# Kernel optimization log

Measured on AMD Instinct MI355X. Metric: run time of the kernel, lower is better.

## Reference

```python
import jax, jax.numpy as jnp
import numpy as np
import math

B, N, C, H, CH = 4, 1024, 512, 8, 64  # batch, seq (Q=K), model dim, heads, head dim

def setup_inputs() -> dict:
    key = jax.random.key(0)
    ks = jax.random.split(key, 11)
    s = 0.02  # small init scale for weights
    f32 = jnp.float32
    return {
        "q_x": jax.random.normal(ks[0], (B, N, C), f32),
        "kv_x": jax.random.normal(ks[1], (B, N, C), f32),
        "bias_mask": jax.random.normal(ks[2], (B, 1, 1, N), f32),
        "bias_pair": jax.random.normal(ks[3], (1, H, N, N), f32),
        "Wq": (jax.random.normal(ks[4], (C, H * CH), f32) * s),
        "Wk": (jax.random.normal(ks[5], (C, H * CH), f32) * s),
        "Wv": (jax.random.normal(ks[6], (C, H * CH), f32) * s),
        "Wg": (jax.random.normal(ks[7], (C, H * CH), f32) * s),
        "bg": jnp.ones((H * CH,), f32),           # 'gating' init: bias=1
        "Wo": (jax.random.normal(ks[8], (H * CH, C), f32) * s),
        "bo": jnp.zeros((C,), f32),               # 'final' init
    }

def reference(q_x, kv_x, bias_mask, bias_pair, Wq, Wk, Wv, Wg, bg, Wo, bo):
    inv_sqrt = 1.0 / math.sqrt(CH)
    # projections -> [B, N, H, CH]
    q = (q_x @ Wq).reshape(B, N, H, CH) * inv_sqrt
    k = (kv_x @ Wk).reshape(B, N, H, CH)
    v = (kv_x @ Wv).reshape(B, N, H, CH)
    # scores [B, H, Q, K] with additive broadcast biases
    scores = jnp.einsum("bqhc,bkhc->bhqk", q, k) + bias_mask + bias_pair
    a = jax.nn.softmax(scores, axis=-1)
    o = jnp.einsum("bhqk,bkhc->bqhc", a, v)  # [B, Q, H, CH]
    # gated output
    g = jax.nn.sigmoid(q_x @ Wg + bg).reshape(B, N, H, CH)
    o = o * g
    out = o.reshape(B, N, H * CH) @ Wo + bo  # [B, Q, C]
    return out
```

## Files before the change

kernel.cpp:

```cpp
#include <hip/hip_runtime.h>
#include <hip/hip_bf16.h>
#include <hip/hip_fp16.h>

#define B_ 4
#define N_ 1024
#define C_ 512
#define H_ 8
#define CH_ 64

typedef _Float16 f16x8 __attribute__((ext_vector_type(8)));
typedef _Float16 f16x4 __attribute__((ext_vector_type(4)));
typedef float f32x4 __attribute__((ext_vector_type(4)));

__global__ void cvt_f32_f16(const float* __restrict__ xq, const float* __restrict__ xkv,
                            _Float16* __restrict__ oq, _Float16* __restrict__ okv) {
  const int n4 = (B_ * N_ * C_) / 4;
  int stride = gridDim.x * blockDim.x;
  for (int idx = blockIdx.x * blockDim.x + threadIdx.x; idx < 2 * n4; idx += stride) {
    const float4* src = (idx < n4) ? (const float4*)xq : (const float4*)xkv;
    _Float16* dst = (idx < n4) ? oq : okv;
    int j = (idx < n4) ? idx : idx - n4;
    float4 v = src[j];
    f16x4 h;
    h[0] = (_Float16)v.x; h[1] = (_Float16)v.y;
    h[2] = (_Float16)v.z; h[3] = (_Float16)v.w;
    *(f16x4*)(dst + (size_t)j * 4) = h;
  }
}

__global__ void transpose_w(const float* __restrict__ Wq, const float* __restrict__ Wk,
                            const float* __restrict__ Wv, const float* __restrict__ Wg,
                            const float* __restrict__ Wo, _Float16* __restrict__ WT) {
  int s = blockIdx.z;
  const float* W = (s == 0) ? Wq : (s == 1) ? Wk : (s == 2) ? Wv : (s == 3) ? Wg : Wo;
  __shared__ float tile[32][33];
  int tx = threadIdx.x & 31, ty = threadIdx.x >> 5;
  int k0 = blockIdx.x * 32, n0 = blockIdx.y * 32;
  #pragma unroll
  for (int r = 0; r < 32; r += 8)
    tile[ty + r][tx] = W[(size_t)(k0 + ty + r) * C_ + n0 + tx];
  __syncthreads();
  _Float16* dst = WT + (size_t)s * C_ * C_;
  #pragma unroll
  for (int r = 0; r < 32; r += 8)
    dst[(size_t)(n0 + ty + r) * C_ + k0 + tx] = (_Float16)tile[tx][ty + r];
}

__global__ __launch_bounds__(256, 2) void proj_gemm(
    const _Float16* __restrict__ xq16, const _Float16* __restrict__ xkv16,
    const _Float16* __restrict__ WT, const float* __restrict__ bg,
    _Float16* __restrict__ Qb, _Float16* __restrict__ Kb,
    _Float16* __restrict__ Vt, float* __restrict__ Gb) {
  int nt0 = blockIdx.x * 128;
  int m0 = blockIdx.y * 128;
  int sel = nt0 >> 9;
  int n0 = nt0 & 511;
  const _Float16* X = (sel == 0 || sel == 3) ? xq16 : xkv16;
  const _Float16* Wt = WT + (size_t)sel * C_ * C_;

  __shared__ __align__(16) char lds[32768];
  char* ldsA = lds;
  char* ldsB = lds + 16384;

  int tid = threadIdx.x;
  int lane = tid & 63, w = tid >> 6;
  int wr = w >> 1, wc = w & 1;
  int lr = lane & 15, lg = lane >> 4;

  f32x4 acc[4][4];
  #pragma unroll
  for (int i = 0; i < 4; i++)
    #pragma unroll
    for (int j = 0; j < 4; j++)
      #pragma unroll
      for (int r = 0; r < 4; r++) acc[i][j][r] = 0.f;

  int srow = tid >> 3, scol = tid & 7;

  for (int k0 = 0; k0 < C_; k0 += 64) {
    __syncthreads();
    #pragma unroll
    for (int p = 0; p < 4; p++) {
      int r = p * 32 + srow;
      *(f16x8*)(ldsA + ((r * 128 + scol * 16) ^ ((r & 7) << 4))) =
          *(const f16x8*)(X + (size_t)(m0 + r) * C_ + k0 + scol * 8);
      *(f16x8*)(ldsB + ((r * 128 + scol * 16) ^ ((r & 7) << 4))) =
          *(const f16x8*)(Wt + (size_t)(n0 + r) * C_ + k0 + scol * 8);
    }
    __syncthreads();
    #pragma unroll
    for (int kh = 0; kh < 2; kh++) {
      f16x8 a[4], b[4];
      #pragma unroll
      for (int i = 0; i < 4; i++) {
        int row = wr * 64 + i * 16 + lr;
        a[i] = *(const f16x8*)(ldsA + ((row * 128 + kh * 64 + lg * 16) ^ ((row & 7) << 4)));
        int col = wc * 64 + i * 16 + lr;
        b[i] = *(const f16x8*)(ldsB + ((col * 128 + kh * 64 + lg * 16) ^ ((col & 7) << 4)));
      }
      #pragma unroll
      for (int i = 0; i < 4; i++)
        #pragma unroll
        for (int j = 0; j < 4; j++)
          acc[i][j] = __builtin_amdgcn_mfma_f32_16x16x32_f16(a[i], b[j], acc[i][j], 0, 0, 0);
    }
  }

  const float inv_sqrt = 0.125f;
  #pragma unroll
  for (int i = 0; i < 4; i++) {
    int token = m0 + wr * 64 + i * 16 + lg * 4;
    #pragma unroll
    for (int j = 0; j < 4; j++) {
      int col = n0 + wc * 64 + j * 16 + lr;
      f32x4 v = acc[i][j];
      if (sel == 0) {
        #pragma unroll
        for (int r = 0; r < 4; r++)
          Qb[(size_t)(token + r) * C_ + col] = (_Float16)(v[r] * inv_sqrt);
      } else if (sel == 1) {
        #pragma unroll
        for (int r = 0; r < 4; r++)
          Kb[(size_t)(token + r) * C_ + col] = (_Float16)v[r];
      } else if (sel == 2) {
        int bb = token >> 10;
        int nn = token & 1023;
        int hh = col >> 6, ch = col & 63;
        f16x4 pk;
        #pragma unroll
        for (int r = 0; r < 4; r++) pk[r] = (_Float16)v[r];
        *(f16x4*)(Vt + (size_t)((bb * H_ + hh) * CH_ + ch) * N_ + nn) = pk;
      } else {
        #pragma unroll
        for (int r = 0; r < 4; r++) {
          float x = v[r] + bg[col];
          Gb[(size_t)(token + r) * C_ + col] = 1.f / (1.f + __expf(-x));
        }
      }
    }
  }
}

__global__ __launch_bounds__(256, 2) void attn(
    const _Float16* __restrict__ Qb, const _Float16* __restrict__ Kb,
    const _Float16* __restrict__ Vt, const float* __restrict__ Gb,
    const float* __restrict__ bias_mask, const float* __restrict__ bias_pair,
    _Float16* __restrict__ Ob) {
  int bid = blockIdx.x;
  int b = bid & 3, h = (bid >> 2) & 7, qt = bid >> 5;
  int q0 = qt * 64;
  int tid = threadIdx.x, lane = tid & 63, w = tid >> 6;
  int lr = lane & 15, lg = lane >> 4;

  __shared__ __align__(16) char lds[49152];
  char* ldsK = lds;
  char* ldsV = lds + 16384;
  char* ldsP = lds + 32768;

  f16x8 qf[2];
  {
    int token = b * N_ + q0 + w * 16 + lr;
    const _Float16* qp = Qb + (size_t)token * C_ + h * CH_;
    qf[0] = *(const f16x8*)(qp + lg * 8);
    qf[1] = *(const f16x8*)(qp + 32 + lg * 8);
  }

  f32x4 acc_o[4];
  #pragma unroll
  for (int j = 0; j < 4; j++)
    #pragma unroll
    for (int r = 0; r < 4; r++) acc_o[j][r] = 0.f;
  float m_run[4], l_run[4];
  #pragma unroll
  for (int r = 0; r < 4; r++) { m_run[r] = -1e30f; l_run[r] = 0.f; }

  int srow = tid >> 3, scol = tid & 7;
  int vrow = tid >> 4, vcol = tid & 15;

  for (int kt = 0; kt < 8; kt++) {
    __syncthreads();
    #pragma unroll
    for (int p = 0; p < 4; p++) {
      int r = p * 32 + srow;
      *(f16x8*)(ldsK + ((r * 128 + scol * 16) ^ ((r & 7) << 4))) =
          *(const f16x8*)(Kb + (size_t)(b * N_ + kt * 128 + r) * C_ + h * CH_ + scol * 8);
    }
    #pragma unroll
    for (int p = 0; p < 4; p++) {
      int r = p * 16 + vrow;
      *(f16x8*)(ldsV + ((r * 256 + vcol * 16) ^ ((r & 7) << 4))) =
          *(const f16x8*)(Vt + (size_t)((b * H_ + h) * CH_ + r) * N_ + kt * 128 + vcol * 8);
    }
    __syncthreads();

    f32x4 s[8];
    #pragma unroll
    for (int ct = 0; ct < 8; ct++) {
      #pragma unroll
      for (int r = 0; r < 4; r++) s[ct][r] = 0.f;
      #pragma unroll
      for (int kh = 0; kh < 2; kh++) {
        int row = ct * 16 + lr;
        f16x8 kf = *(const f16x8*)(ldsK + ((row * 128 + kh * 64 + lg * 16) ^ ((row & 7) << 4)));
        s[ct] = __builtin_amdgcn_mfma_f32_16x16x32_f16(qf[kh], kf, s[ct], 0, 0, 0);
      }
    }
    int qrow = q0 + w * 16 + lg * 4;
    #pragma unroll
    for (int ct = 0; ct < 8; ct++) {
      float bm = bias_mask[b * N_ + kt * 128 + ct * 16 + lr];
      const float* bp = bias_pair + ((size_t)h * N_ + qrow) * N_ + kt * 128 + ct * 16 + lr;
      #pragma unroll
      for (int r = 0; r < 4; r++) s[ct][r] += bm + bp[(size_t)r * N_];
    }
    #pragma unroll
    for (int r = 0; r < 4; r++) {
      float mx = s[0][r];
      #pragma unroll
      for (int ct = 1; ct < 8; ct++) mx = fmaxf(mx, s[ct][r]);
      #pragma unroll
      for (int o = 1; o < 16; o <<= 1) mx = fmaxf(mx, __shfl_xor(mx, o, 64));
      float m_new = fmaxf(m_run[r], mx);
      float sc = __expf(m_run[r] - m_new);
      m_run[r] = m_new;
      float sum = 0.f;
      #pragma unroll
      for (int ct = 0; ct < 8; ct++) {
        float p = __expf(s[ct][r] - m_new);
        s[ct][r] = p;
        sum += p;
      }
      #pragma unroll
      for (int o = 1; o < 16; o <<= 1) sum += __shfl_xor(sum, o, 64);
      l_run[r] = l_run[r] * sc + sum;
      #pragma unroll
      for (int j = 0; j < 4; j++) acc_o[j][r] *= sc;
    }
    char* myP = ldsP + w * 4096;
    #pragma unroll
    for (int ct = 0; ct < 8; ct++) {
      #pragma unroll
      for (int r = 0; r < 4; r++) {
        int row = lg * 4 + r;
        *(_Float16*)(myP + ((row * 256 + (ct * 16 + lr) * 2) ^ ((row & 7) << 4))) =
            (_Float16)s[ct][r];
      }
    }
    #pragma unroll
    for (int ks = 0; ks < 4; ks++) {
      f16x8 pf = *(const f16x8*)(myP + ((lr * 256 + ks * 64 + lg * 16) ^ ((lr & 7) << 4)));
      #pragma unroll
      for (int cc = 0; cc < 4; cc++) {
        int vr = cc * 16 + lr;
        f16x8 vf = *(const f16x8*)(ldsV + ((vr * 256 + ks * 64 + lg * 16) ^ ((vr & 7) << 4)));
        acc_o[cc] = __builtin_amdgcn_mfma_f32_16x16x32_f16(pf, vf, acc_o[cc], 0, 0, 0);
      }
    }
  }

  #pragma unroll
  for (int cc = 0; cc < 4; cc++) {
    #pragma unroll
    for (int r = 0; r < 4; r++) {
      int token = b * N_ + q0 + w * 16 + lg * 4 + r;
      int col = h * CH_ + cc * 16 + lr;
      float o = acc_o[cc][r] / l_run[r];
      float gv = Gb[(size_t)token * C_ + col];
      Ob[(size_t)token * C_ + col] = (_Float16)(o * gv);
    }
  }
}

__global__ __launch_bounds__(256, 2) void out_gemm(
    const _Float16* __restrict__ Ob, const _Float16* __restrict__ WTo,
    const float* __restrict__ bo, float* __restrict__ out) {
  int n0 = blockIdx.x * 128;
  int m0 = blockIdx.y * 128;
  __shared__ __align__(16) char lds[32768];
  char* ldsA = lds;
  char* ldsB = lds + 16384;
  int tid = threadIdx.x;
  int lane = tid & 63, w = tid >> 6;
  int wr = w >> 1, wc = w & 1;
  int lr = lane & 15, lg = lane >> 4;
  f32x4 acc[4][4];
  #pragma unroll
  for (int i = 0; i < 4; i++)
    #pragma unroll
    for (int j = 0; j < 4; j++)
      #pragma unroll
      for (int r = 0; r < 4; r++) acc[i][j][r] = 0.f;
  int srow = tid >> 3, scol = tid & 7;
  for (int k0 = 0; k0 < C_; k0 += 64) {
    __syncthreads();
    #pragma unroll
    for (int p = 0; p < 4; p++) {
      int r = p * 32 + srow;
      *(f16x8*)(ldsA + ((r * 128 + scol * 16) ^ ((r & 7) << 4))) =
          *(const f16x8*)(Ob + (size_t)(m0 + r) * C_ + k0 + scol * 8);
      *(f16x8*)(ldsB + ((r * 128 + scol * 16) ^ ((r & 7) << 4))) =
          *(const f16x8*)(WTo + (size_t)(n0 + r) * C_ + k0 + scol * 8);
    }
    __syncthreads();
    #pragma unroll
    for (int kh = 0; kh < 2; kh++) {
      f16x8 a[4], bfr[4];
      #pragma unroll
      for (int i = 0; i < 4; i++) {
        int row = wr * 64 + i * 16 + lr;
        a[i] = *(const f16x8*)(ldsA + ((row * 128 + kh * 64 + lg * 16) ^ ((row & 7) << 4)));
        int col = wc * 64 + i * 16 + lr;
        bfr[i] = *(const f16x8*)(ldsB + ((col * 128 + kh * 64 + lg * 16) ^ ((col & 7) << 4)));
      }
      #pragma unroll
      for (int i = 0; i < 4; i++)
        #pragma unroll
        for (int j = 0; j < 4; j++)
          acc[i][j] = __builtin_amdgcn_mfma_f32_16x16x32_f16(a[i], bfr[j], acc[i][j], 0, 0, 0);
    }
  }
  #pragma unroll
  for (int i = 0; i < 4; i++) {
    int token = m0 + wr * 64 + i * 16 + lg * 4;
    #pragma unroll
    for (int j = 0; j < 4; j++) {
      int col = n0 + wc * 64 + j * 16 + lr;
      float bb = bo[col];
      #pragma unroll
      for (int r = 0; r < 4; r++)
        out[(size_t)(token + r) * C_ + col] = acc[i][j][r] + bb;
    }
  }
}

extern "C" void kernel_launch(void* const* d_in, const int* in_sizes, int n_in,
                              void* d_out, int out_size, void* d_ws, size_t ws_size,
                              hipStream_t stream) {
  const float* q_x = (const float*)d_in[0];
  const float* kv_x = (const float*)d_in[1];
  const float* bias_mask = (const float*)d_in[2];
  const float* bias_pair = (const float*)d_in[3];
  const float* Wq = (const float*)d_in[4];
  const float* Wk = (const float*)d_in[5];
  const float* Wv = (const float*)d_in[6];
  const float* Wg = (const float*)d_in[7];
  const float* bg = (const float*)d_in[8];
  const float* Wo = (const float*)d_in[9];
  const float* bo = (const float*)d_in[10];
  float* out = (float*)d_out;

  char* ws = (char*)d_ws;
  const size_t MB = 1024 * 1024;
  _Float16* xq16 = (_Float16*)(ws + 0);
  _Float16* xkv16 = (_Float16*)(ws + 4 * MB);
  _Float16* WT = (_Float16*)(ws + 8 * MB);
  _Float16* Qb = (_Float16*)(ws + 11 * MB);
  _Float16* Kb = (_Float16*)(ws + 15 * MB);
  _Float16* Vt = (_Float16*)(ws + 19 * MB);
  float* Gb = (float*)(ws + 23 * MB);
  _Float16* Ob = (_Float16*)(ws + 31 * MB);

  cvt_f32_f16<<<2048, 256, 0, stream>>>(q_x, kv_x, xq16, xkv16);
  transpose_w<<<dim3(16, 16, 5), 256, 0, stream>>>(Wq, Wk, Wv, Wg, Wo, WT);
  proj_gemm<<<dim3(16, 32), 256, 0, stream>>>(xq16, xkv16, WT, bg, Qb, Kb, Vt, Gb);
  attn<<<512, 256, 0, stream>>>(Qb, Kb, Vt, Gb, bias_mask, bias_pair, Ob);
  out_gemm<<<dim3(4, 32), 256, 0, stream>>>(Ob, WT + 4 * (size_t)C_ * C_, bo, out);
}
```

Baseline: 83.15 us.

## Transpose attention MFMA layout, prefetch K/V tiles, vectorize bias loads, store gate as fp16

The attention kernel swaps the MFMA operand order so each lane holds one query row across key columns. This turns the softmax row reductions into two cross-group shuffles with one running max/sum per lane, and lets bias_pair be read as float4 vectors along the key dimension. K/V tiles for the next step are loaded into registers while the current step computes. The gate buffer is stored in fp16 and read as vectors in the epilogue, and block indexing now groups the 8 heads of a batch/query tile next to each other. Together these aim to cut bias-load and reduction overhead and to hide global latency, at the cost of higher register pressure and fp16 rounding of the gate.

```diff
diff --git a/kernel.cpp b/kernel.cpp
--- a/kernel.cpp
+++ b/kernel.cpp
@@ -50,7 +50,7 @@
     const _Float16* __restrict__ xq16, const _Float16* __restrict__ xkv16,
     const _Float16* __restrict__ WT, const float* __restrict__ bg,
     _Float16* __restrict__ Qb, _Float16* __restrict__ Kb,
-    _Float16* __restrict__ Vt, float* __restrict__ Gb) {
+    _Float16* __restrict__ Vt, _Float16* __restrict__ Gb) {
   int nt0 = blockIdx.x * 128;
   int m0 = blockIdx.y * 128;
   int sel = nt0 >> 9;
@@ -134,7 +134,7 @@
         #pragma unroll
         for (int r = 0; r < 4; r++) {
           float x = v[r] + bg[col];
-          Gb[(size_t)(token + r) * C_ + col] = 1.f / (1.f + __expf(-x));
+          Gb[(size_t)(token + r) * C_ + col] = (_Float16)(1.f / (1.f + __expf(-x)));
         }
       }
     }
@@ -143,11 +143,11 @@
 
 __global__ __launch_bounds__(256, 2) void attn(
     const _Float16* __restrict__ Qb, const _Float16* __restrict__ Kb,
-    const _Float16* __restrict__ Vt, const float* __restrict__ Gb,
+    const _Float16* __restrict__ Vt, const _Float16* __restrict__ Gb,
     const float* __restrict__ bias_mask, const float* __restrict__ bias_pair,
     _Float16* __restrict__ Ob) {
   int bid = blockIdx.x;
-  int b = bid & 3, h = (bid >> 2) & 7, qt = bid >> 5;
+  int h = bid & 7, b = (bid >> 3) & 3, qt = bid >> 5;
   int q0 = qt * 64;
   int tid = threadIdx.x, lane = tid & 63, w = tid >> 6;
   int lr = lane & 15, lg = lane >> 4;
@@ -170,29 +170,46 @@
   for (int j = 0; j < 4; j++)
     #pragma unroll
     for (int r = 0; r < 4; r++) acc_o[j][r] = 0.f;
-  float m_run[4], l_run[4];
-  #pragma unroll
-  for (int r = 0; r < 4; r++) { m_run[r] = -1e30f; l_run[r] = 0.f; }
+  float m_run = -1e30f, l_run = 0.f;
 
   int srow = tid >> 3, scol = tid & 7;
   int vrow = tid >> 4, vcol = tid & 15;
 
+  const _Float16* Kbase = Kb + (size_t)(b * N_) * C_ + h * CH_;
+  const _Float16* Vbase = Vt + (size_t)((b * H_ + h) * CH_) * N_;
+
+  f16x8 kr[4], vr[4];
+  #pragma unroll
+  for (int p = 0; p < 4; p++) {
+    kr[p] = *(const f16x8*)(Kbase + (size_t)(p * 32 + srow) * C_ + scol * 8);
+    vr[p] = *(const f16x8*)(Vbase + (size_t)(p * 16 + vrow) * N_ + vcol * 8);
+  }
+
   for (int kt = 0; kt < 8; kt++) {
     __syncthreads();
     #pragma unroll
     for (int p = 0; p < 4; p++) {
       int r = p * 32 + srow;
-      *(f16x8*)(ldsK + ((r * 128 + scol * 16) ^ ((r & 7) << 4))) =
-          *(const f16x8*)(Kb + (size_t)(b * N_ + kt * 128 + r) * C_ + h * CH_ + scol * 8);
-    }
-    #pragma unroll
-    for (int p = 0; p < 4; p++) {
-      int r = p * 16 + vrow;
-      *(f16x8*)(ldsV + ((r * 256 + vcol * 16) ^ ((r & 7) << 4))) =
-          *(const f16x8*)(Vt + (size_t)((b * H_ + h) * CH_ + r) * N_ + kt * 128 + vcol * 8);
-    }
-    __syncthreads();
-
+      *(f16x8*)(ldsK + ((r * 128 + scol * 16) ^ ((r & 7) << 4))) = kr[p];
+      int rv = p * 16 + vrow;
+      *(f16x8*)(ldsV + ((rv * 256 + vcol * 16) ^ ((rv & 7) << 4))) = vr[p];
+    }
+    __syncthreads();
+    if (kt < 7) {
+      #pragma unroll
+      for (int p = 0; p < 4; p++) {
+        kr[p] = *(const f16x8*)(Kbase + (size_t)((kt + 1) * 128 + p * 32 + srow) * C_ + scol * 8);
+        vr[p] = *(const f16x8*)(Vbase + (size_t)(p * 16 + vrow) * N_ + (kt + 1) * 128 + vcol * 8);
+      }
+    }
+    f32x4 bias[8];
+    {
+      const float* bp = bias_pair + ((size_t)h * N_ + q0 + w * 16 + lr) * N_ + kt * 128 + lg * 4;
+      const float* bm = bias_mask + b * N_ + kt * 128 + lg * 4;
+      #pragma unroll
+      for (int ct = 0; ct < 8; ct++)
+        bias[ct] = *(const f32x4*)(bp + ct * 16) + *(const f32x4*)(bm + ct * 16);
+    }
     f32x4 s[8];
     #pragma unroll
     for (int ct = 0; ct < 8; ct++) {
@@ -202,71 +219,68 @@
       for (int kh = 0; kh < 2; kh++) {
         int row = ct * 16 + lr;
         f16x8 kf = *(const f16x8*)(ldsK + ((row * 128 + kh * 64 + lg * 16) ^ ((row & 7) << 4)));
-        s[ct] = __builtin_amdgcn_mfma_f32_16x16x32_f16(qf[kh], kf, s[ct], 0, 0, 0);
-      }
-    }
-    int qrow = q0 + w * 16 + lg * 4;
-    #pragma unroll
-    for (int ct = 0; ct < 8; ct++) {
-      float bm = bias_mask[b * N_ + kt * 128 + ct * 16 + lr];
-      const float* bp = bias_pair + ((size_t)h * N_ + qrow) * N_ + kt * 128 + ct * 16 + lr;
-      #pragma unroll
-      for (int r = 0; r < 4; r++) s[ct][r] += bm + bp[(size_t)r * N_];
-    }
-    #pragma unroll
-    for (int r = 0; r < 4; r++) {
-      float mx = s[0][r];
-      #pragma unroll
-      for (int ct = 1; ct < 8; ct++) mx = fmaxf(mx, s[ct][r]);
-      #pragma unroll
-      for (int o = 1; o < 16; o <<= 1) mx = fmaxf(mx, __shfl_xor(mx, o, 64));
-      float m_new = fmaxf(m_run[r], mx);
-      float sc = __expf(m_run[r] - m_new);
-      m_run[r] = m_new;
-      float sum = 0.f;
-      #pragma unroll
-      for (int ct = 0; ct < 8; ct++) {
+        s[ct] = __builtin_amdgcn_mfma_f32_16x16x32_f16(kf, qf[kh], s[ct], 0, 0, 0);
+      }
+      s[ct] += bias[ct];
+    }
+    float mx = s[0][0];
+    #pragma unroll
+    for (int ct = 0; ct < 8; ct++)
+      #pragma unroll
+      for (int r = 0; r < 4; r++) mx = fmaxf(mx, s[ct][r]);
+    mx = fmaxf(mx, __shfl_xor(mx, 16, 64));
+    mx = fmaxf(mx, __shfl_xor(mx, 32, 64));
+    float m_new = fmaxf(m_run, mx);
+    float sc = __expf(m_run - m_new);
+    m_run = m_new;
+    float sum = 0.f;
+    #pragma unroll
+    for (int ct = 0; ct < 8; ct++)
+      #pragma unroll
+      for (int r = 0; r < 4; r++) {
         float p = __expf(s[ct][r] - m_new);
         s[ct][r] = p;
         sum += p;
       }
-      #pragma unroll
-      for (int o = 1; o < 16; o <<= 1) sum += __shfl_xor(sum, o, 64);
-      l_run[r] = l_run[r] * sc + sum;
-      #pragma unroll
-      for (int j = 0; j < 4; j++) acc_o[j][r] *= sc;
-    }
+    sum += __shfl_xor(sum, 16, 64);
+    sum += __shfl_xor(sum, 32, 64);
+    l_run = l_run * sc + sum;
+    #pragma unroll
+    for (int j = 0; j < 4; j++)
+      #pragma unroll
+      for (int r = 0; r < 4; r++) acc_o[j][r] *= sc;
     char* myP = ldsP + w * 4096;
     #pragma unroll
     for (int ct = 0; ct < 8; ct++) {
-      #pragma unroll
-      for (int r = 0; r < 4; r++) {
-        int row = lg * 4 + r;
-        *(_Float16*)(myP + ((row * 256 + (ct * 16 + lr) * 2) ^ ((row & 7) << 4))) =
-            (_Float16)s[ct][r];
-      }
+      f16x4 pk;
+      #pragma unroll
+      for (int r = 0; r < 4; r++) pk[r] = (_Float16)s[ct][r];
+      *(f16x4*)(myP + ((lr * 256 + ct * 32 + lg * 8) ^ ((lr & 7) << 4))) = pk;
     }
     #pragma unroll
     for (int ks = 0; ks < 4; ks++) {
       f16x8 pf = *(const f16x8*)(myP + ((lr * 256 + ks * 64 + lg * 16) ^ ((lr & 7) << 4)));
       #pragma unroll
       for (int cc = 0; cc < 4; cc++) {
-        int vr = cc * 16 + lr;
-        f16x8 vf = *(const f16x8*)(ldsV + ((vr * 256 + ks * 64 + lg * 16) ^ ((vr & 7) << 4)));
-        acc_o[cc] = __builtin_amdgcn_mfma_f32_16x16x32_f16(pf, vf, acc_o[cc], 0, 0, 0);
-      }
-    }
-  }
-
-  #pragma unroll
-  for (int cc = 0; cc < 4; cc++) {
-    #pragma unroll
-    for (int r = 0; r < 4; r++) {
-      int token = b * N_ + q0 + w * 16 + lg * 4 + r;
-      int col = h * CH_ + cc * 16 + lr;
-      float o = acc_o[cc][r] / l_run[r];
-      float gv = Gb[(size_t)token * C_ + col];
-      Ob[(size_t)token * C_ + col] = (_Float16)(o * gv);
+        int vrr = cc * 16 + lr;
+        f16x8 vf = *(const f16x8*)(ldsV + ((vrr * 256 + ks * 64 + lg * 16) ^ ((vrr & 7) << 4)));
+        acc_o[cc] = __builtin_amdgcn_mfma_f32_16x16x32_f16(vf, pf, acc_o[cc], 0, 0, 0);
+      }
+    }
+  }
+
+  {
+    int token = b * N_ + q0 + w * 16 + lr;
+    float inv_l = 1.f / l_run;
+    #pragma unroll
+    for (int cc = 0; cc < 4; cc++) {
+      int col = h * CH_ + cc * 16 + lg * 4;
+      f16x4 g4 = *(const f16x4*)(Gb + (size_t)token * C_ + col);
+      f16x4 o4;
+      #pragma unroll
+      for (int r = 0; r < 4; r++)
+        o4[r] = (_Float16)(acc_o[cc][r] * inv_l * (float)g4[r]);
+      *(f16x4*)(Ob + (size_t)token * C_ + col) = o4;
     }
   }
 }
@@ -357,7 +371,7 @@
   _Float16* Qb = (_Float16*)(ws + 11 * MB);
   _Float16* Kb = (_Float16*)(ws + 15 * MB);
   _Float16* Vt = (_Float16*)(ws + 19 * MB);
-  float* Gb = (float*)(ws + 23 * MB);
+  _Float16* Gb = (_Float16*)(ws + 23 * MB);
   _Float16* Ob = (_Float16*)(ws + 31 * MB);
 
   cvt_f32_f16<<<2048, 256, 0, stream>>>(q_x, kv_x, xq16, xkv16);
```

Measured after the change: 77.21 us. 7.2% less time.
